# Kernel optimization log

Measured on AMD Instinct MI355X. Metric: run time of the kernel, lower is better.

## Reference

```python
import jax, jax.numpy as jnp
import numpy as np

D_MODEL = 512
N_HEADS = 8
HEAD_DIM = D_MODEL // N_HEADS
D_FF = 2048
RADIUS = 1                      # manhattan_radius
MAX_LEVEL = 2                   # layer_max_level
WINDOWS = (512, 64, 16)         # window_size_per_level


def _layer_norm(x, g, b, eps=1e-5):
    mu = jnp.mean(x, axis=-1, keepdims=True)
    var = jnp.mean(jnp.square(x - mu), axis=-1, keepdims=True)
    return (x - mu) * jax.lax.rsqrt(var + eps) * g + b


def setup_inputs() -> dict:
    key = jax.random.key(0)
    ks = jax.random.split(key, 16)
    B, N = 2, 2048
    s = 0.02
    return {
        "x": jax.random.normal(ks[0], (B, N, D_MODEL), jnp.float32),
        "coords_pos": jax.random.randint(ks[1], (B, N, 2), 0, 64, jnp.int32),
        "coords_level": jax.random.randint(ks[2], (B, N), 0, 3, jnp.int32),
        "w_qkv": jax.random.normal(ks[3], (D_MODEL, 3 * D_MODEL), jnp.float32) * s,
        "b_qkv": jnp.zeros((3 * D_MODEL,), jnp.float32),
        "w_out": jax.random.normal(ks[4], (D_MODEL, D_MODEL), jnp.float32) * s,
        "b_out": jnp.zeros((D_MODEL,), jnp.float32),
        "w_ff1": jax.random.normal(ks[5], (D_MODEL, D_FF), jnp.float32) * s,
        "b_ff1": jnp.zeros((D_FF,), jnp.float32),
        "w_ff2": jax.random.normal(ks[6], (D_FF, D_MODEL), jnp.float32) * s,
        "b_ff2": jnp.zeros((D_MODEL,), jnp.float32),
        "ln1_g": jnp.ones((D_MODEL,), jnp.float32),
        "ln1_b": jnp.zeros((D_MODEL,), jnp.float32),
        "ln2_g": jnp.ones((D_MODEL,), jnp.float32),
        "ln2_b": jnp.zeros((D_MODEL,), jnp.float32),
    }


def _geometric_mask(coords_pos, coords_level):
    """[B,N,N] bool mask: same hierarchy level, Manhattan distance <= RADIUS,
    within the per-level sequence window, levels <= MAX_LEVEL; self always allowed."""
    B, N = coords_level.shape
    # Manhattan distance on grid coords  [B,N,N]
    dist = jnp.sum(jnp.abs(coords_pos[:, :, None, :] - coords_pos[:, None, :, :]), axis=-1)
    same_level = coords_level[:, :, None] == coords_level[:, None, :]
    lvl_ok = coords_level <= MAX_LEVEL                       # [B,N]
    lvl_pair = lvl_ok[:, :, None] & lvl_ok[:, None, :]
    win_tab = jnp.array(WINDOWS, jnp.int32)
    win_q = win_tab[jnp.clip(coords_level, 0, len(WINDOWS) - 1)]  # [B,N]
    idx = jnp.arange(N, dtype=jnp.int32)
    seq_dist = jnp.abs(idx[:, None] - idx[None, :])          # [N,N]
    in_window = seq_dist[None] < win_q[:, :, None]
    eye = jnp.eye(N, dtype=bool)[None]
    return (same_level & (dist <= RADIUS) & in_window & lvl_pair) | eye


def reference(x, coords_pos, coords_level, w_qkv, b_qkv, w_out, b_out,
              w_ff1, b_ff1, w_ff2, b_ff2, ln1_g, ln1_b, ln2_g, ln2_b):
    B, N, D = x.shape
    residual = x
    xn = _layer_norm(x, ln1_g, ln1_b)
    qkv = (xn @ w_qkv + b_qkv).reshape(B, N, 3, N_HEADS, HEAD_DIM)
    q, k, v = qkv[:, :, 0], qkv[:, :, 1], qkv[:, :, 2]        # [B,N,H,Dh]

    scale = 1.0 / np.sqrt(HEAD_DIM)
    scores = jnp.einsum("bihd,bjhd->bhij", q, k) * scale      # [B,H,N,N]
    mask = _geometric_mask(coords_pos, coords_level)          # [B,N,N]
    scores = jnp.where(mask[:, None], scores, jnp.float32(-1e9))
    probs = jax.nn.softmax(scores, axis=-1)
    attn = jnp.einsum("bhij,bjhd->bihd", probs, v).reshape(B, N, D)
    x = residual + (attn @ w_out + b_out)                     # dropout = identity (eval)

    residual = x
    xn = _layer_norm(x, ln2_g, ln2_b)
    h = jax.nn.gelu(xn @ w_ff1 + b_ff1, approximate=False)
    x = residual + (h @ w_ff2 + b_ff2)
    return x
```

## Files before the change

kernel.cpp:

```cpp
#include <hip/hip_runtime.h>
#include <hip/hip_bf16.h>

#define DMODEL 512
#define NHEADS 8
#define DFF 2048
#define NSEQ 2048
#define NROWS 4096

typedef __attribute__((ext_vector_type(8))) short   bf16x8;
typedef __attribute__((ext_vector_type(4))) float   f32x4;
typedef __attribute__((ext_vector_type(8))) unsigned short u16x8;

__device__ __forceinline__ unsigned short f2bf(float f) {
  union { float f; unsigned u; } v; v.f = f;
  unsigned r = v.u + 0x7fffu + ((v.u >> 16) & 1u);
  return (unsigned short)(r >> 16);
}
__device__ __forceinline__ float bf2f(unsigned short u) {
  union { unsigned u; float f; } v; v.u = (unsigned)u << 16;
  return v.f;
}

#define GLL16(src, dst) \
  __builtin_amdgcn_global_load_lds((__attribute__((address_space(1))) const void*)(src), \
                                   (__attribute__((address_space(3))) void*)(dst), 16, 0, 0)

__global__ __launch_bounds__(256)
void prep(const float* __restrict__ w_qkv, const float* __restrict__ w_out,
          const float* __restrict__ w_ff1, const float* __restrict__ w_ff2,
          const float* __restrict__ ln1_g, const float* __restrict__ ln1_b,
          const float* __restrict__ ln2_g, const float* __restrict__ ln2_b,
          const float* __restrict__ b_qkv, const float* __restrict__ b_ff1,
          const float* __restrict__ x,
          unsigned short* __restrict__ wqkvT, unsigned short* __restrict__ woutT,
          unsigned short* __restrict__ wff1T, unsigned short* __restrict__ wff2T,
          float* __restrict__ vq, float* __restrict__ uq,
          float* __restrict__ vf, float* __restrict__ uf,
          unsigned short* __restrict__ x_bf, float2* __restrict__ stats1,
          float* __restrict__ stats2) {
  __shared__ char smem_raw[12288];
  int bid = blockIdx.x;
  const int tid = threadIdx.x;
  if (bid < 3072) {
    unsigned short (*t)[33] = (unsigned short (*)[33])smem_raw;
    const float* w; unsigned short* wT; const float* g; int K, N;
    if (bid < 768)       { w = w_qkv; wT = wqkvT; g = ln1_g; K = 512;  N = 1536; }
    else if (bid < 1024) { bid -= 768;  w = w_out; wT = woutT; g = nullptr; K = 512;  N = 512; }
    else if (bid < 2048) { bid -= 1024; w = w_ff1; wT = wff1T; g = ln2_g; K = 512;  N = 2048; }
    else                 { bid -= 2048; w = w_ff2; wT = wff2T; g = nullptr; K = 2048; N = 512; }
    const int ntx = N >> 5;
    const int n0 = (bid % ntx) * 32, k0 = (bid / ntx) * 32;
    const int tx = tid & 31, ty = tid >> 5;
    #pragma unroll
    for (int i = 0; i < 4; ++i) {
      const int k = k0 + ty + i * 8;
      const float s = g ? g[k] : 1.0f;
      t[ty + i * 8][tx] = f2bf(s * w[(size_t)k * N + n0 + tx]);
    }
    __syncthreads();
    #pragma unroll
    for (int i = 0; i < 4; ++i)
      wT[(size_t)(n0 + ty + i * 8) * K + k0 + tx] = t[tx][ty + i * 8];
  } else if (bid < 3100) {
    const int b = bid - 3072;
    const float *w, *g, *bb, *bias; float *ov, *ou; int N, n0;
    if (b < 12) { w = w_qkv; g = ln1_g; bb = ln1_b; bias = b_qkv;
                  ov = vq; ou = uq; N = 1536; n0 = b * 128; }
    else        { w = w_ff1; g = ln2_g; bb = ln2_b; bias = b_ff1;
                  ov = vf; ou = uf; N = 2048; n0 = (b - 12) * 128; }
    float*  sg = (float*)smem_raw;
    float*  sb = sg + 512;
    float4* pu = (float4*)(sb + 512);
    float4* pv = pu + 256;
    sg[tid] = g[tid];  sg[tid + 256] = g[tid + 256];
    sb[tid] = bb[tid]; sb[tid + 256] = bb[tid + 256];
    __syncthreads();
    const int c4 = tid & 31, kg = tid >> 5;
    float4 su = make_float4(0, 0, 0, 0), sv = make_float4(0, 0, 0, 0);
    const float* wp = w + (size_t)(kg * 64) * N + n0 + c4 * 4;
    #pragma unroll 8
    for (int kk = 0; kk < 64; ++kk) {
      const float4 wv = *(const float4*)(wp + (size_t)kk * N);
      const float gk = sg[kg * 64 + kk], bk = sb[kg * 64 + kk];
      su.x = fmaf(bk, wv.x, su.x); su.y = fmaf(bk, wv.y, su.y);
      su.z = fmaf(bk, wv.z, su.z); su.w = fmaf(bk, wv.w, su.w);
      sv.x = fmaf(gk, wv.x, sv.x); sv.y = fmaf(gk, wv.y, sv.y);
      sv.z = fmaf(gk, wv.z, sv.z); sv.w = fmaf(gk, wv.w, sv.w);
    }
    pu[kg * 32 + c4] = su; pv[kg * 32 + c4] = sv;
    __syncthreads();
    if (tid < 32) {
      float4 u = pu[tid], v = pv[tid];
      #pragma unroll
      for (int q = 1; q < 8; ++q) {
        const float4 a = pu[q * 32 + tid], c = pv[q * 32 + tid];
        u.x += a.x; u.y += a.y; u.z += a.z; u.w += a.w;
        v.x += c.x; v.y += c.y; v.z += c.z; v.w += c.w;
      }
      const float4 bv = *(const float4*)(bias + n0 + tid * 4);
      u.x += bv.x; u.y += bv.y; u.z += bv.z; u.w += bv.w;
      *(float4*)(ov + n0 + tid * 4) = v;
      *(float4*)(ou + n0 + tid * 4) = u;
    }
  } else if (bid < 4124) {
    const int row = (bid - 3100) * 4 + (tid >> 6);
    const int lane = tid & 63;
    const float* xr = x + (size_t)row * DMODEL + lane * 8;
    const float4 v0 = *(const float4*)(xr);
    const float4 v1 = *(const float4*)(xr + 4);
    float s  = v0.x + v0.y + v0.z + v0.w + v1.x + v1.y + v1.z + v1.w;
    float s2 = v0.x*v0.x + v0.y*v0.y + v0.z*v0.z + v0.w*v0.w
             + v1.x*v1.x + v1.y*v1.y + v1.z*v1.z + v1.w*v1.w;
    #pragma unroll
    for (int m = 1; m < 64; m <<= 1) {
      s  += __shfl_xor(s,  m);
      s2 += __shfl_xor(s2, m);
    }
    const float mu  = s * (1.0f / DMODEL);
    const float var = s2 * (1.0f / DMODEL) - mu * mu;
    const float rs  = rsqrtf(var + 1e-5f);
    if (lane == 0) stats1[row] = make_float2(mu, rs);
    u16x8 o;
    o[0] = f2bf(v0.x); o[1] = f2bf(v0.y); o[2] = f2bf(v0.z); o[3] = f2bf(v0.w);
    o[4] = f2bf(v1.x); o[5] = f2bf(v1.y); o[6] = f2bf(v1.z); o[7] = f2bf(v1.w);
    *(u16x8*)(x_bf + (size_t)row * DMODEL + lane * 8) = o;
  } else {
    const int idx = (bid - 4124) * 256 + tid;
    if (idx < 2 * NROWS) stats2[idx] = 0.0f;
  }
}

template<int MODE>
__global__ __launch_bounds__(256)
void gemm128(const unsigned short* __restrict__ A,
             const unsigned short* __restrict__ Bt,
             const float* __restrict__ v, const float* __restrict__ u,
             const float* __restrict__ stats, unsigned short* __restrict__ Cb,
             int M, int N, int LDA, int KL) {
  __shared__ unsigned short As[2][128 * 64];
  __shared__ unsigned short Bs[2][128 * 64];

  const int tid = threadIdx.x;
  const int w = tid >> 6, l = tid & 63;
  const int gx = N >> 7;
  const int nxy = gx * (M >> 7);
  int lin = blockIdx.x;
  lin = (lin & 7) * (nxy >> 3) + (lin >> 3);
  const int bn = (lin % gx) << 7;
  const int bm = (lin / gx) << 7;
  const int wr = (w >> 1) * 64;
  const int wc = (w & 1) * 64;
  const int lr = l & 15, kg = l >> 4;

  f32x4 acc[4][4] = {};

  auto stage = [&](int buf, int k0) {
    #pragma unroll
    for (int i = 0; i < 4; ++i) {
      const int g = i * 4 + w;
      const int c = g * 64 + l;
      const int row = c >> 3;
      const int kc = (c & 7) ^ (row & 7);
      GLL16(A + (size_t)(bm + row) * LDA + k0 + kc * 8, &As[buf][g * 512]);
    }
    #pragma unroll
    for (int i = 0; i < 4; ++i) {
      const int g = i * 4 + w;
      const int c = g * 64 + l;
      const int row = c >> 3;
      const int kc = (c & 7) ^ (row & 7);
      GLL16(Bt + (size_t)(bn + row) * LDA + k0 + kc * 8, &Bs[buf][g * 512]);
    }
  };

  const int nt = KL >> 6;
  stage(0, 0);
  for (int t = 0; t < nt; ++t) {
    asm volatile("s_waitcnt vmcnt(0)" ::: "memory");
    __builtin_amdgcn_sched_barrier(0);
    __builtin_amdgcn_s_barrier();
    __builtin_amdgcn_sched_barrier(0);
    if (t + 1 < nt) stage((t + 1) & 1, (t + 1) << 6);
    const int cur = t & 1;
    #pragma unroll
    for (int ks = 0; ks < 2; ++ks) {
      const int cc = ks * 4 + kg;
      bf16x8 af[4], bfv[4];
      #pragma unroll
      for (int mi = 0; mi < 4; ++mi) {
        const int row = wr + mi * 16 + lr;
        af[mi] = *(const bf16x8*)&As[cur][(row * 8 + (cc ^ (row & 7))) * 8];
      }
      #pragma unroll
      for (int ni = 0; ni < 4; ++ni) {
        const int row = wc + ni * 16 + lr;
        bfv[ni] = *(const bf16x8*)&Bs[cur][(row * 8 + (cc ^ (row & 7))) * 8];
      }
      __builtin_amdgcn_s_setprio(1);
      #pragma unroll
      for (int mi = 0; mi < 4; ++mi)
        #pragma unroll
        for (int ni = 0; ni < 4; ++ni)
          acc[mi][ni] = __builtin_amdgcn_mfma_f32_16x16x32_bf16(
              af[mi], bfv[ni], acc[mi][ni], 0, 0, 0);
      __builtin_amdgcn_s_setprio(0);
    }
    __builtin_amdgcn_s_barrier();
  }

  __syncthreads();
  float* sc = ((float*)&As[0][0]) + w * (64 * 36);
  const int r2 = l >> 2, ch = l & 3, c0 = ch * 8;
  #pragma unroll
  for (int p = 0; p < 2; ++p) {
    #pragma unroll
    for (int mi = 0; mi < 4; ++mi)
      #pragma unroll
      for (int ni = 0; ni < 2; ++ni)
        #pragma unroll
        for (int reg = 0; reg < 4; ++reg)
          sc[(mi * 16 + kg * 4 + reg) * 36 + ni * 16 + lr] = acc[mi][p * 2 + ni][reg];
    #pragma unroll
    for (int i2 = 0; i2 < 4; ++i2) {
      const int rl = i2 * 16 + r2;
      const int grow = bm + wr + rl;
      const int gcol = bn + wc + p * 32 + c0;
      const float4 va = *(const float4*)&sc[rl * 36 + c0];
      const float4 vb = *(const float4*)&sc[rl * 36 + c0 + 4];
      float vals[8] = {va.x, va.y, va.z, va.w, vb.x, vb.y, vb.z, vb.w};
      float mu, rs;
      if (MODE == 4) {
        const float2 st = ((const float2*)stats)[grow];
        mu = st.x; rs = st.y;
      } else {
        const float2 st = ((const float2*)stats)[grow];
        mu = st.x * (1.0f / DMODEL);
        rs = rsqrtf(st.y * (1.0f / DMODEL) - mu * mu + 1e-5f);
      }
      const float4 v0 = *(const float4*)&v[gcol];
      const float4 v1 = *(const float4*)&v[gcol + 4];
      const float4 u0 = *(const float4*)&u[gcol];
      const float4 u1 = *(const float4*)&u[gcol + 4];
      const float vv[8] = {v0.x, v0.y, v0.z, v0.w, v1.x, v1.y, v1.z, v1.w};
      const float uu[8] = {u0.x, u0.y, u0.z, u0.w, u1.x, u1.y, u1.z, u1.w};
      u16x8 o;
      #pragma unroll
      for (int e = 0; e < 8; ++e) {
        float t = rs * (vals[e] - mu * vv[e]) + uu[e];
        if (MODE == 6) t = 0.5f * t * (1.0f + erff(t * 0.70710678118654752f));
        o[e] = f2bf(t);
      }
      *(u16x8*)&Cb[(size_t)grow * N + gcol] = o;
    }
    if (p == 0) __builtin_amdgcn_s_barrier();
  }
}

template<int MODE, int BM>
__global__ __launch_bounds__(256)
void gemm_bf16(const unsigned short* __restrict__ A,
               const unsigned short* __restrict__ Bt,
               const float* __restrict__ bias,
               const float* __restrict__ resf, const unsigned short* __restrict__ resb,
               float* __restrict__ stats, void* __restrict__ Cout,
               int M, int N, int LDA, int KL) {
  constexpr int MR = BM / 32;
  constexpr int PS = BM / 32 + 2;
  constexpr int ROWS = BM / 2;
  __shared__ unsigned short As[3][BM * 64];
  __shared__ unsigned short Bs[3][64 * 64];

  const int tid = threadIdx.x;
  const int w = tid >> 6, l = tid & 63;
  const int gx = N >> 6;
  const int nxy = gx * (M / BM);
  int lin = blockIdx.x;
  lin = (lin & 7) * (nxy >> 3) + (lin >> 3);
  const int bn = (lin % gx) << 6;
  const int bm = (lin / gx) * BM;
  const int wr = (w >> 1) * (BM >> 1);
  const int wc = (w & 1) * 32;
  const int lr = l & 15, kg = l >> 4;

  f32x4 acc[MR][2] = {};

  auto stage = [&](int buf, int k0) {
    #pragma unroll
    for (int i = 0; i < BM / 32; ++i) {
      const int g = i * 4 + w;
      const int c = g * 64 + l;
      const int row = c >> 3;
      const int kc = (c & 7) ^ (row & 7);
      GLL16(A + (size_t)(bm + row) * LDA + k0 + kc * 8, &As[buf][g * 512]);
    }
    #pragma unroll
    for (int i = 0; i < 2; ++i) {
      const int g = i * 4 + w;
      const int c = g * 64 + l;
      const int row = c >> 3;
      const int kc = (c & 7) ^ (row & 7);
      GLL16(Bt + (size_t)(bn + row) * LDA + k0 + kc * 8, &Bs[buf][g * 512]);
    }
  };

  const int nt = KL >> 6;
  stage(0, 0);
  stage(1, 64);
  for (int t = 0; t < nt; ++t) {
    if (t + 1 < nt) {
      asm volatile("s_waitcnt vmcnt(%0)" :: "n"(PS) : "memory");
    } else {
      asm volatile("s_waitcnt vmcnt(0)" ::: "memory");
    }
    __builtin_amdgcn_sched_barrier(0);
    __builtin_amdgcn_s_barrier();
    __builtin_amdgcn_sched_barrier(0);
    if (t + 2 < nt) stage((t + 2) % 3, (t + 2) << 6);
    const int cur = t % 3;
    #pragma unroll
    for (int ks = 0; ks < 2; ++ks) {
      const int cc = ks * 4 + kg;
      bf16x8 af[MR], bfv[2];
      #pragma unroll
      for (int mi = 0; mi < MR; ++mi) {
        const int row = wr + mi * 16 + lr;
        af[mi] = *(const bf16x8*)&As[cur][(row * 8 + (cc ^ (row & 7))) * 8];
      }
      #pragma unroll
      for (int ni = 0; ni < 2; ++ni) {
        const int row = wc + ni * 16 + lr;
        bfv[ni] = *(const bf16x8*)&Bs[cur][(row * 8 + (cc ^ (row & 7))) * 8];
      }
      __builtin_amdgcn_s_setprio(1);
      #pragma unroll
      for (int mi = 0; mi < MR; ++mi)
        #pragma unroll
        for (int ni = 0; ni < 2; ++ni)
          acc[mi][ni] = __builtin_amdgcn_mfma_f32_16x16x32_bf16(
              af[mi], bfv[ni], acc[mi][ni], 0, 0, 0);
      __builtin_amdgcn_s_setprio(0);
    }
  }

  __syncthreads();
  float* sc = ((float*)&As[0][0]) + w * (ROWS * 36);
  #pragma unroll
  for (int mi = 0; mi < MR; ++mi)
    #pragma unroll
    for (int ni = 0; ni < 2; ++ni)
      #pragma unroll
      for (int reg = 0; reg < 4; ++reg)
        sc[(mi * 16 + kg * 4 + reg) * 36 + ni * 16 + lr] = acc[mi][ni][reg];

  float* Cf = (float*)Cout;
  unsigned short* Cb = (unsigned short*)Cout;
  const int r2 = l >> 2, ch = l & 3;
  #pragma unroll
  for (int i2 = 0; i2 < ROWS / 16; ++i2) {
    const int rl = i2 * 16 + r2;
    const int grow = bm + wr + rl;
    const int c0 = ch * 8;
    const int gcol = bn + wc + c0;
    const float4 va = *(const float4*)&sc[rl * 36 + c0];
    const float4 vb = *(const float4*)&sc[rl * 36 + c0 + 4];
    float vals[8] = {va.x, va.y, va.z, va.w, vb.x, vb.y, vb.z, vb.w};

    if (MODE == 5) {
      const float4 b0 = *(const float4*)&bias[gcol];
      const float4 b1 = *(const float4*)&bias[gcol + 4];
      const float4 r0 = *(const float4*)&resf[(size_t)grow * N + gcol];
      const float4 r1 = *(const float4*)&resf[(size_t)grow * N + gcol + 4];
      const float bb[8] = {b0.x, b0.y, b0.z, b0.w, b1.x, b1.y, b1.z, b1.w};
      const float rr[8] = {r0.x, r0.y, r0.z, r0.w, r1.x, r1.y, r1.z, r1.w};
      float rsum = 0.0f, rsq = 0.0f;
      u16x8 o;
      #pragma unroll
      for (int e = 0; e < 8; ++e) {
        const float t = vals[e] + bb[e] + rr[e];
        o[e] = f2bf(t);
        rsum += t; rsq = fmaf(t, t, rsq);
      }
      *(u16x8*)&Cb[(size_t)grow * N + gcol] = o;
      rsum += __shfl_xor(rsum, 1); rsq += __shfl_xor(rsq, 1);
      rsum += __shfl_xor(rsum, 2); rsq += __shfl_xor(rsq, 2);
      if (ch == 0) {
        atomicAdd(&stats[2 * grow],     rsum);
        atomicAdd(&stats[2 * grow + 1], rsq);
      }
    }

    if (MODE == 7) {
      const float4 b0 = *(const float4*)&bias[gcol];
      const float4 b1 = *(const float4*)&bias[gcol + 4];
      const u16x8 rb = *(const u16x8*)&resb[(size_t)grow * N + gcol];
      const float bb[8] = {b0.x, b0.y, b0.z, b0.w, b1.x, b1.y, b1.z, b1.w};
      #pragma unroll
      for (int e = 0; e < 8; ++e) vals[e] += bb[e] + bf2f(rb[e]);
      *(float4*)&Cf[(size_t)grow * N + gcol] =
          make_float4(vals[0], vals[1], vals[2], vals[3]);
      *(float4*)&Cf[(size_t)grow * N + gcol + 4] =
          make_float4(vals[4], vals[5], vals[6], vals[7]);
    }
  }
}

#define CAP 256
__global__ __launch_bounds__(64)
void attn_kernel(const unsigned short* __restrict__ qkv,
                 const int* __restrict__ pos, const int* __restrict__ lvl,
                 unsigned short* __restrict__ out) {
  const int bid = blockIdx.x;
  const int r = (bid & 7) * (NROWS / 8) + (bid >> 3);
  const int i = r & (NSEQ - 1);
  const int base = r - i;
  const int lane = threadIdx.x;

  __shared__ int   s_idx[CAP];
  __shared__ int   s_cnt;
  __shared__ float s_sc[NHEADS][CAP];
  __shared__ float s_inv[NHEADS];

  if (lane == 0) s_cnt = 0;
  __syncthreads();

  const int li = lvl[r];
  const int2 pq = *(const int2*)(pos + 2 * r);
  const int win = (li == 0) ? 512 : (li == 1 ? 64 : 16);
  const int jlo = max(i - win + 1, 0);
  const int jhi = min(i + win - 1, NSEQ - 1);

  for (int j = jlo + lane; j <= jhi; j += 64) {
    const int rj = base + j;
    bool m = (j == i);
    if (!m) {
      const int lj = lvl[rj];
      const int2 pj = *(const int2*)(pos + 2 * rj);
      const int d = abs(pq.x - pj.x) + abs(pq.y - pj.y);
      m = (lj == li) && (d <= 1);
    }
    if (m) {
      const int p = atomicAdd(&s_cnt, 1);
      if (p < CAP) s_idx[p] = j;
    }
  }
  __syncthreads();
  const int cnt = min(s_cnt, CAP);

  const u16x8 qv = *(const u16x8*)(qkv + (size_t)r * 1536 + lane * 8);
  float qf[8];
  #pragma unroll
  for (int e = 0; e < 8; ++e) qf[e] = bf2f(qv[e]);

  for (int jj = 0; jj < cnt; ++jj) {
    const int rj = base + s_idx[jj];
    const u16x8 kv = *(const u16x8*)(qkv + (size_t)rj * 1536 + 512 + lane * 8);
    float p = 0.0f;
    #pragma unroll
    for (int e = 0; e < 8; ++e) p = fmaf(qf[e], bf2f(kv[e]), p);
    p += __shfl_xor(p, 1);
    p += __shfl_xor(p, 2);
    p += __shfl_xor(p, 4);
    if ((lane & 7) == 0) s_sc[lane >> 3][jj] = p * 0.125f;
  }
  __syncthreads();

  if (lane < 8) {
    float mx = -1e30f;
    for (int jj = 0; jj < cnt; ++jj) mx = fmaxf(mx, s_sc[lane][jj]);
    float den = 0.0f;
    for (int jj = 0; jj < cnt; ++jj) {
      const float e = expf(s_sc[lane][jj] - mx);
      s_sc[lane][jj] = e;
      den += e;
    }
    s_inv[lane] = 1.0f / den;
  }
  __syncthreads();

  const int h = lane >> 3;
  float a[8] = {};
  for (int jj = 0; jj < cnt; ++jj) {
    const float pp = s_sc[h][jj];
    const u16x8 vv = *(const u16x8*)(qkv + (size_t)(base + s_idx[jj]) * 1536 + 1024 + lane * 8);
    #pragma unroll
    for (int e = 0; e < 8; ++e) a[e] = fmaf(pp, bf2f(vv[e]), a[e]);
  }
  const float inv = s_inv[h];
  u16x8 o;
  #pragma unroll
  for (int e = 0; e < 8; ++e) o[e] = f2bf(a[e] * inv);
  *(u16x8*)(out + (size_t)r * DMODEL + lane * 8) = o;
}

extern "C" void kernel_launch(void* const* d_in, const int* in_sizes, int n_in,
                              void* d_out, int out_size, void* d_ws, size_t ws_size,
                              hipStream_t stream) {
  const float* x            = (const float*)d_in[0];
  const int*   coords_pos   = (const int*)d_in[1];
  const int*   coords_level = (const int*)d_in[2];
  const float* w_qkv        = (const float*)d_in[3];
  const float* b_qkv        = (const float*)d_in[4];
  const float* w_out        = (const float*)d_in[5];
  const float* b_out        = (const float*)d_in[6];
  const float* w_ff1        = (const float*)d_in[7];
  const float* b_ff1        = (const float*)d_in[8];
  const float* w_ff2        = (const float*)d_in[9];
  const float* b_ff2        = (const float*)d_in[10];
  const float* ln1_g        = (const float*)d_in[11];
  const float* ln1_b        = (const float*)d_in[12];
  const float* ln2_g        = (const float*)d_in[13];
  const float* ln2_b        = (const float*)d_in[14];
  float* out = (float*)d_out;

  char* ws = (char*)d_ws;
  unsigned short* qkv_bf = (unsigned short*)(ws);
  unsigned short* h_bf   = (unsigned short*)(ws);
  unsigned short* x_bf   = (unsigned short*)(ws + 16777216);
  unsigned short* at_bf  = (unsigned short*)(ws + 20971520);
  unsigned short* x1_bf  = (unsigned short*)(ws + 25165824);
  unsigned short* wqkvT  = (unsigned short*)(ws + 29360128);
  unsigned short* woutT  = (unsigned short*)(ws + 30932992);
  unsigned short* wff1T  = (unsigned short*)(ws + 31457280);
  unsigned short* wff2T  = (unsigned short*)(ws + 33554432);
  float*          vq     = (float*)(ws + 35651584);
  float*          uq     = (float*)(ws + 35657728);
  float*          vf     = (float*)(ws + 35663872);
  float*          uf     = (float*)(ws + 35672064);
  float2*         stats1 = (float2*)(ws + 35680256);
  float*          stats2 = (float*)(ws + 35713024);

  prep<<<4156, 256, 0, stream>>>(w_qkv, w_out, w_ff1, w_ff2,
                                 ln1_g, ln1_b, ln2_g, ln2_b, b_qkv, b_ff1, x,
                                 wqkvT, woutT, wff1T, wff2T,
                                 vq, uq, vf, uf, x_bf, stats1, stats2);

  gemm128<4><<<(1536/128)*(NROWS/128), 256, 0, stream>>>(
      x_bf, wqkvT, vq, uq, (const float*)stats1, qkv_bf, NROWS, 1536, DMODEL, DMODEL);

  attn_kernel<<<NROWS, 64, 0, stream>>>(qkv_bf, coords_pos, coords_level, at_bf);

  gemm_bf16<5, 64><<<(DMODEL/64)*(NROWS/64), 256, 0, stream>>>(
      at_bf, woutT, b_out, x, nullptr, stats2, x1_bf, NROWS, DMODEL, DMODEL, DMODEL);

  gemm128<6><<<(DFF/128)*(NROWS/128), 256, 0, stream>>>(
      x1_bf, wff1T, vf, uf, stats2, h_bf, NROWS, DFF, DMODEL, DMODEL);

  gemm_bf16<7, 64><<<(DMODEL/64)*(NROWS/64), 256, 0, stream>>>(
      h_bf, wff2T, b_ff2, nullptr, x1_bf, nullptr, out, NROWS, DMODEL, DFF, DFF);
}
```

Baseline: 92.21 us.

## Switch gemm128 to triple-buffered BK=32 pipeline with partial vmcnt waits

Changes the GEMM main loop from double-buffered 64-wide K tiles to triple-buffered 32-wide K tiles, keeping two stages of loads in flight and waiting only on the older one (vmcnt(4)). The trailing barrier per iteration is dropped since the three-slot ring ensures a buffer is not overwritten while being read. LDS use falls to 48 KB and launch bounds request 3 blocks per CU, aiming for more occupancy and better latency hiding. In exchange there are twice as many barriers and loop iterations, with less MFMA work between them, and the swizzle drops to a 4-chunk XOR that may cause more LDS bank conflicts.

```diff
diff --git a/kernel.cpp b/kernel.cpp
--- a/kernel.cpp
+++ b/kernel.cpp
@@ -131,14 +131,13 @@
 }
 
 template<int MODE>
-__global__ __launch_bounds__(256)
+__global__ __launch_bounds__(256, 3)
 void gemm128(const unsigned short* __restrict__ A,
              const unsigned short* __restrict__ Bt,
              const float* __restrict__ v, const float* __restrict__ u,
              const float* __restrict__ stats, unsigned short* __restrict__ Cb,
              int M, int N, int LDA, int KL) {
-  __shared__ unsigned short As[2][128 * 64];
-  __shared__ unsigned short Bs[2][128 * 64];
+  __shared__ unsigned short smem[24576];
 
   const int tid = threadIdx.x;
   const int w = tid >> 6, l = tid & 63;
@@ -155,61 +154,64 @@
   f32x4 acc[4][4] = {};
 
   auto stage = [&](int buf, int k0) {
-    #pragma unroll
-    for (int i = 0; i < 4; ++i) {
+    unsigned short* As = smem + buf * 4096;
+    unsigned short* Bs = smem + 12288 + buf * 4096;
+    #pragma unroll
+    for (int i = 0; i < 2; ++i) {
       const int g = i * 4 + w;
       const int c = g * 64 + l;
-      const int row = c >> 3;
-      const int kc = (c & 7) ^ (row & 7);
-      GLL16(A + (size_t)(bm + row) * LDA + k0 + kc * 8, &As[buf][g * 512]);
-    }
-    #pragma unroll
-    for (int i = 0; i < 4; ++i) {
+      const int row = c >> 2;
+      const int kc = (c & 3) ^ (row & 3);
+      GLL16(A + (size_t)(bm + row) * LDA + k0 + kc * 8, As + g * 512);
+    }
+    #pragma unroll
+    for (int i = 0; i < 2; ++i) {
       const int g = i * 4 + w;
       const int c = g * 64 + l;
-      const int row = c >> 3;
-      const int kc = (c & 7) ^ (row & 7);
-      GLL16(Bt + (size_t)(bn + row) * LDA + k0 + kc * 8, &Bs[buf][g * 512]);
+      const int row = c >> 2;
+      const int kc = (c & 3) ^ (row & 3);
+      GLL16(Bt + (size_t)(bn + row) * LDA + k0 + kc * 8, Bs + g * 512);
     }
   };
 
-  const int nt = KL >> 6;
+  const int nt = KL >> 5;
   stage(0, 0);
+  stage(1, 32);
   for (int t = 0; t < nt; ++t) {
-    asm volatile("s_waitcnt vmcnt(0)" ::: "memory");
+    if (t + 1 < nt) {
+      asm volatile("s_waitcnt vmcnt(4)" ::: "memory");
+    } else {
+      asm volatile("s_waitcnt vmcnt(0)" ::: "memory");
+    }
     __builtin_amdgcn_sched_barrier(0);
     __builtin_amdgcn_s_barrier();
     __builtin_amdgcn_sched_barrier(0);
-    if (t + 1 < nt) stage((t + 1) & 1, (t + 1) << 6);
-    const int cur = t & 1;
-    #pragma unroll
-    for (int ks = 0; ks < 2; ++ks) {
-      const int cc = ks * 4 + kg;
-      bf16x8 af[4], bfv[4];
-      #pragma unroll
-      for (int mi = 0; mi < 4; ++mi) {
-        const int row = wr + mi * 16 + lr;
-        af[mi] = *(const bf16x8*)&As[cur][(row * 8 + (cc ^ (row & 7))) * 8];
-      }
-      #pragma unroll
-      for (int ni = 0; ni < 4; ++ni) {
-        const int row = wc + ni * 16 + lr;
-        bfv[ni] = *(const bf16x8*)&Bs[cur][(row * 8 + (cc ^ (row & 7))) * 8];
-      }
-      __builtin_amdgcn_s_setprio(1);
-      #pragma unroll
-      for (int mi = 0; mi < 4; ++mi)
-        #pragma unroll
-        for (int ni = 0; ni < 4; ++ni)
-          acc[mi][ni] = __builtin_amdgcn_mfma_f32_16x16x32_bf16(
-              af[mi], bfv[ni], acc[mi][ni], 0, 0, 0);
-      __builtin_amdgcn_s_setprio(0);
-    }
-    __builtin_amdgcn_s_barrier();
+    if (t + 2 < nt) stage((t + 2) % 3, (t + 2) << 5);
+    const unsigned short* As = smem + (t % 3) * 4096;
+    const unsigned short* Bs = smem + 12288 + (t % 3) * 4096;
+    bf16x8 af[4], bfv[4];
+    #pragma unroll
+    for (int mi = 0; mi < 4; ++mi) {
+      const int row = wr + mi * 16 + lr;
+      af[mi] = *(const bf16x8*)&As[(row * 4 + (kg ^ (row & 3))) * 8];
+    }
+    #pragma unroll
+    for (int ni = 0; ni < 4; ++ni) {
+      const int row = wc + ni * 16 + lr;
+      bfv[ni] = *(const bf16x8*)&Bs[(row * 4 + (kg ^ (row & 3))) * 8];
+    }
+    __builtin_amdgcn_s_setprio(1);
+    #pragma unroll
+    for (int mi = 0; mi < 4; ++mi)
+      #pragma unroll
+      for (int ni = 0; ni < 4; ++ni)
+        acc[mi][ni] = __builtin_amdgcn_mfma_f32_16x16x32_bf16(
+            af[mi], bfv[ni], acc[mi][ni], 0, 0, 0);
+    __builtin_amdgcn_s_setprio(0);
   }
 
   __syncthreads();
-  float* sc = ((float*)&As[0][0]) + w * (64 * 36);
+  float* sc = ((float*)smem) + w * (64 * 36);
   const int r2 = l >> 2, ch = l & 3, c0 = ch * 8;
   #pragma unroll
   for (int p = 0; p < 2; ++p) {
```

Result: no change. 92.18 us (-0.0%).
